# Kernel optimization log

Hardware: AMD Instinct MI355X
Metric: run time of the kernel (lower is better)

Reference implementation:

```python
import jax, jax.numpy as jnp
import numpy as np

N = 250_000          # num nodes
E = 2_000_000        # undirected edges -> 2E directed edges
C = 2                # num_class
POT = 0.95           # self potential
THRESH = 1e-6
MAX_ITERS = 10


def setup_inputs() -> dict:
    key = jax.random.key(0)
    k1, k2, k3 = jax.random.split(key, 3)
    u = jax.random.randint(k1, (E,), 0, N)
    v = jax.random.randint(k2, (E,), 0, N)
    # directed edge list: first E edges u->v, next E edges v->u
    src_nodes = jnp.concatenate([u, v]).astype(jnp.int64)
    dst_nodes = jnp.concatenate([v, u]).astype(jnp.int64)
    # reverse-edge index: edge i (<E) reverses to i+E and vice versa
    ar = jnp.arange(E, dtype=jnp.int64)
    rev_edges = jnp.concatenate([ar + E, ar])
    # strictly positive class priors, rows sum to 1
    priors = jax.nn.softmax(jax.random.normal(k3, (N, C), dtype=jnp.float32), axis=1)
    return {"priors": priors, "src_nodes": src_nodes,
            "dst_nodes": dst_nodes, "rev_edges": rev_edges}


def _potential_matrix(dtype):
    off = (1.0 - POT) / C * (C - 1)
    diag = POT / C
    P = jnp.full((C, C), off, dtype=dtype)
    return P.at[jnp.arange(C), jnp.arange(C)].set(diag)


def reference(priors, src_nodes, dst_nodes, rev_edges):
    P = _potential_matrix(priors.dtype)
    log_priors = jnp.log(priors)
    n_dir = src_nodes.shape[0]  # 2E directed edges
    messages0 = jnp.full((n_dir, C), 0.5, dtype=priors.dtype)

    def update_messages(messages, beliefs):
        # gather beliefs at edge sources, divide by reverse messages, CxC matmul
        m = (beliefs[src_nodes] / messages[rev_edges]) @ P  # [2E, C]
        return m / jnp.sum(m, axis=1, keepdims=True)

    def compute_beliefs(messages):
        b = log_priors.at[dst_nodes].add(jnp.log(messages))  # scatter-add
        return jax.nn.softmax(b, axis=1)

    def cond(state):
        i, beliefs, messages, diff = state
        return jnp.logical_and(i < MAX_ITERS, diff >= THRESH)

    def body(state):
        i, beliefs, messages, _ = state
        new_m = update_messages(messages, beliefs)
        new_b = compute_beliefs(new_m)
        diff = jnp.max(jnp.abs(new_b - beliefs))
        return (i + 1, new_b, new_m, diff)

    init = (jnp.array(0, jnp.int32), priors, messages0,
            jnp.array(jnp.inf, priors.dtype))
    _, beliefs, _, _ = jax.lax.while_loop(cond, body, init)
    return beliefs
```

## Files before the change

kernel.cpp:

```cpp
#include <hip/hip_runtime.h>
#include <hip/hip_fp16.h>


#define POT_D 0.475f
#define POT_O 0.025f

constexpr int BKT_SHIFT = 8;
constexpr int BKT_NODES = 1 << BKT_SHIFT;
constexpr int GB = 512;
constexpr int ITEMS = GB / 64;
constexpr int FB = 512;
constexpr int T = 9;

__device__ __forceinline__ float pot_logit(float x) {
  float t = __expf(-fabsf(x));
  float v = __logf((POT_D + POT_O * t) / (POT_O + POT_D * t));
  return copysignf(v, x);
}

__global__ void init_nodes(const float* __restrict__ priors, float* __restrict__ lpd, int N) {
  int n = blockIdx.x * blockDim.x + threadIdx.x;
  if (n < N) {
    float2 p = reinterpret_cast<const float2*>(priors)[n];
    lpd[n] = __logf(p.x) - __logf(p.y);
  }
}

__global__ void rank_kernel(const int* __restrict__ dst, int* __restrict__ blkhist,
                            int* __restrict__ rnk, int M, int NB, int CH) {
  extern __shared__ int h[];
  for (int i = threadIdx.x; i < NB; i += blockDim.x) h[i] = 0;
  __syncthreads();
  int s = blockIdx.x * CH, e1 = min(s + CH, M);
  for (int e = s + threadIdx.x; e < e1; e += blockDim.x)
    rnk[e] = atomicAdd(&h[dst[e] >> BKT_SHIFT], 1);
  __syncthreads();
  for (int i = threadIdx.x; i < NB; i += blockDim.x)
    blkhist[(size_t)i * GB + blockIdx.x] = h[i];
}

__global__ void colscan_kernel(int* __restrict__ blkhist, int* __restrict__ deg, int NB) {
  int wave = (blockIdx.x * blockDim.x + threadIdx.x) >> 6;
  int lane = threadIdx.x & 63;
  if (wave >= NB) return;
  int* row = blkhist + (size_t)wave * GB;
  int v[ITEMS];
  int s = 0;
#pragma unroll
  for (int j = 0; j < ITEMS; ++j) { v[j] = row[ITEMS * lane + j]; s += v[j]; }
  int tot = s;
  for (int off = 1; off < 64; off <<= 1) {
    int t = __shfl_up(tot, off, 64);
    if (lane >= off) tot += t;
  }
  int excl = tot - s;
#pragma unroll
  for (int j = 0; j < ITEMS; ++j) { int t = v[j]; row[ITEMS * lane + j] = excl; excl += t; }
  if (lane == 63) deg[wave] = tot;
}

__global__ void scan_kernel(const int* __restrict__ deg, int* __restrict__ base,
                            int NB, int M) {
  __shared__ int s[1024];
  __shared__ int carry;
  int tid = threadIdx.x;
  if (tid == 0) carry = 0;
  __syncthreads();
  for (int c = 0; c < NB; c += 1024) {
    int v = (c + tid < NB) ? deg[c + tid] : 0;
    s[tid] = v;
    __syncthreads();
    for (int off = 1; off < 1024; off <<= 1) {
      int t = (tid >= off) ? s[tid - off] : 0;
      __syncthreads();
      s[tid] += t;
      __syncthreads();
    }
    if (c + tid < NB) base[c + tid] = carry + s[tid] - v;
    __syncthreads();
    if (tid == 0) carry += s[1023];
    __syncthreads();
  }
  if (tid == 0) base[NB] = M;
}

__global__ void place_kernel(const int* __restrict__ dst, const int* __restrict__ blkhist,
                             const int* __restrict__ base, const int* __restrict__ rnk,
                             int* __restrict__ posof, int M, int NB, int CH) {
  extern __shared__ int cur[];
  for (int i = threadIdx.x; i < NB; i += blockDim.x)
    cur[i] = base[i] + blkhist[(size_t)i * GB + blockIdx.x];
  __syncthreads();
  int s = blockIdx.x * CH, e1 = min(s + CH, M);
  for (int e = s + threadIdx.x; e < e1; e += blockDim.x)
    posof[e] = cur[dst[e] >> BKT_SHIFT] + rnk[e];
}

__global__ void pass2_kernel(const int* __restrict__ dst, const int* __restrict__ posof,
                             unsigned* __restrict__ g2, int M, int E, int CH) {
  int s = blockIdx.x * CH, e1 = min(s + CH, M);
  for (int e = s + threadIdx.x; e < e1; e += blockDim.x) {
    int r = (e < E) ? (e + E) : (e - E);
    unsigned loc = (unsigned)(dst[e] & (BKT_NODES - 1));
    g2[posof[e]] = (loc << 24) | (unsigned)posof[r];
  }
}

__global__ void initcav_kernel(const unsigned* __restrict__ g2, const int* __restrict__ base,
                               const float* __restrict__ lpd, __half* __restrict__ cav) {
  int b = blockIdx.x;
  int rs = base[b], re = base[b + 1];
  for (int k = rs + threadIdx.x; k < re; k += blockDim.x) {
    int node = (b << BKT_SHIFT) | (int)(g2[k] >> 24);
    cav[k] = __float2half(lpd[node]);
  }
}

__global__ void F_kernel(const unsigned* __restrict__ g2, const int* __restrict__ base,
                         const float* __restrict__ lpd, const __half* __restrict__ cin,
                         __half* __restrict__ cout, int N) {
  __shared__ float zb[BKT_NODES];
  __shared__ float zl[BKT_NODES];
  int b = blockIdx.x;
  int rs = base[b], re = base[b + 1];
  if (threadIdx.x < BKT_NODES) zb[threadIdx.x] = 0.0f;
  __syncthreads();
  if (re > rs) {
    int k0 = rs + threadIdx.x;
    unsigned w[T];
    float L[T];
#pragma unroll
    for (int j = 0; j < T; ++j)
      w[j] = g2[min(k0 + j * FB, re - 1)];
#pragma unroll
    for (int j = 0; j < T; ++j)
      L[j] = __half2float(cin[w[j] & 0xFFFFFFu]);
#pragma unroll
    for (int j = 0; j < T; ++j) {
      L[j] = pot_logit(L[j]);
      if (k0 + j * FB < re) atomicAdd(&zb[w[j] >> 24], L[j]);
    }
    for (int k = k0 + T * FB; k < re; k += FB)
      { unsigned w2 = g2[k]; atomicAdd(&zb[w2 >> 24], pot_logit(__half2float(cin[w2 & 0xFFFFFFu]))); }
    __syncthreads();
    if (threadIdx.x < BKT_NODES) {
      int node = (b << BKT_SHIFT) + threadIdx.x;
      zl[threadIdx.x] = (node < N ? lpd[node] : 0.0f) + zb[threadIdx.x];
    }
    __syncthreads();
#pragma unroll
    for (int j = 0; j < T; ++j) {
      int k = k0 + j * FB;
      if (k < re) cout[k] = __float2half(zl[w[j] >> 24] - L[j]);
    }
    for (int k = k0 + T * FB; k < re; k += FB)
      { unsigned w2 = g2[k]; cout[k] = __float2half(zl[w2 >> 24] - pot_logit(__half2float(cin[w2 & 0xFFFFFFu]))); }
  }
}

__global__ void out_kernel(const unsigned* __restrict__ g2, const int* __restrict__ base,
                           const float* __restrict__ lpd, const __half* __restrict__ cin,
                           float2* __restrict__ out, int N) {
  __shared__ float zb[BKT_NODES];
  int b = blockIdx.x;
  int rs = base[b], re = base[b + 1];
  if (threadIdx.x < BKT_NODES) zb[threadIdx.x] = 0.0f;
  __syncthreads();
  int k0 = rs + threadIdx.x;
  if (re > rs) {
    unsigned w[T];
    float c[T];
#pragma unroll
    for (int j = 0; j < T; ++j)
      w[j] = g2[min(k0 + j * FB, re - 1)];
#pragma unroll
    for (int j = 0; j < T; ++j)
      c[j] = __half2float(cin[w[j] & 0xFFFFFFu]);
#pragma unroll
    for (int j = 0; j < T; ++j)
      if (k0 + j * FB < re) atomicAdd(&zb[w[j] >> 24], pot_logit(c[j]));
    for (int k = k0 + T * FB; k < re; k += FB)
      { unsigned w2 = g2[k]; atomicAdd(&zb[w2 >> 24], pot_logit(__half2float(cin[w2 & 0xFFFFFFu]))); }
  }
  __syncthreads();
  int node = (b << BKT_SHIFT) + threadIdx.x;
  if (threadIdx.x < BKT_NODES && node < N) {
    float z = lpd[node] + zb[threadIdx.x];
    float p = 1.0f / (1.0f + __expf(-z));
    out[node] = make_float2(p, 1.0f - p);
  }
}

extern "C" void kernel_launch(void* const* d_in, const int* in_sizes, int n_in,
                              void* d_out, int out_size, void* d_ws, size_t ws_size,
                              hipStream_t stream) {
  const float* priors = (const float*)d_in[0];
  const int* dst = (const int*)d_in[2];
  const int N = in_sizes[0] / 2;
  const int M = in_sizes[1];
  const int E = M / 2;
  const int NB = (N + BKT_NODES - 1) / BKT_NODES;
  const int CH = (M + GB - 1) / GB;

  float* ws = (float*)d_ws;
  float* lpd = ws;
  unsigned* g2 = (unsigned*)(ws + N);
  int* rnk = (int*)(ws + N + (size_t)M);
  int* posof = (int*)(ws + N + 2 * (size_t)M);
  __half* cavA = (__half*)(ws + N + 3 * (size_t)M);
  __half* cavB = cavA + M;
  int* blkhist = (int*)(ws + N + 4 * (size_t)M);
  int* deg = blkhist + (size_t)NB * GB;
  int* base = deg + NB;

  const int B = 256;
  init_nodes<<<(N + B - 1) / B, B, 0, stream>>>(priors, lpd, N);
  rank_kernel<<<GB, B, NB * sizeof(int), stream>>>(dst, blkhist, rnk, M, NB, CH);
  colscan_kernel<<<(NB * 64 + B - 1) / B, B, 0, stream>>>(blkhist, deg, NB);
  scan_kernel<<<1, 1024, 0, stream>>>(deg, base, NB, M);
  place_kernel<<<GB, B, NB * sizeof(int), stream>>>(dst, blkhist, base, rnk, posof, M, NB, CH);
  pass2_kernel<<<GB, B, 0, stream>>>(dst, posof, g2, M, E, CH);
  initcav_kernel<<<NB, B, 0, stream>>>(g2, base, lpd, cavA);

  __half* bufs[2] = {cavA, cavB};
  for (int t = 0; t < 9; ++t)
    F_kernel<<<NB, FB, 0, stream>>>(g2, base, lpd, bufs[t & 1], bufs[1 - (t & 1)], N);
  out_kernel<<<NB, FB, 0, stream>>>(g2, base, lpd, cavB, (float2*)d_out, N);
}
```

Measured before the change: 576.3 us.

## Fuse BP iterations into one persistent cooperative kernel with grid syncs

Replaces the init-cavity kernel, the nine per-iteration F kernels and the output kernel with a single cooperative kernel. It loops over buckets with a fixed grid of 512 blocks and uses grid.sync between iterations, removing repeated kernel launch overhead and tail gaps. The pass2 launch geometry is also changed to fewer, larger blocks. The cost is that each block now handles about two buckets in sequence, which gives some load imbalance. It also adds grid-wide barrier costs and the occupancy limit of a cooperative launch.

```diff
diff --git a/kernel.cpp b/kernel.cpp
--- a/kernel.cpp
+++ b/kernel.cpp
@@ -1,5 +1,8 @@
 #include <hip/hip_runtime.h>
 #include <hip/hip_fp16.h>
+#include <hip/hip_cooperative_groups.h>
+
+namespace cg = cooperative_groups;
 
 
 #define POT_D 0.475f
@@ -8,8 +11,10 @@
 constexpr int BKT_SHIFT = 8;
 constexpr int BKT_NODES = 1 << BKT_SHIFT;
 constexpr int GB = 512;
+constexpr int GB2 = 128;
 constexpr int ITEMS = GB / 64;
 constexpr int FB = 512;
+constexpr int GRID = 512;
 constexpr int T = 9;
 
 __device__ __forceinline__ float pot_logit(float x) {
@@ -97,8 +102,8 @@
 }
 
 __global__ void pass2_kernel(const int* __restrict__ dst, const int* __restrict__ posof,
-                             unsigned* __restrict__ g2, int M, int E, int CH) {
-  int s = blockIdx.x * CH, e1 = min(s + CH, M);
+                             unsigned* __restrict__ g2, int M, int E, int CH2) {
+  int s = blockIdx.x * CH2, e1 = min(s + CH2, M);
   for (int e = s + threadIdx.x; e < e1; e += blockDim.x) {
     int r = (e < E) ? (e + E) : (e - E);
     unsigned loc = (unsigned)(dst[e] & (BKT_NODES - 1));
@@ -106,88 +111,95 @@
   }
 }
 
-__global__ void initcav_kernel(const unsigned* __restrict__ g2, const int* __restrict__ base,
-                               const float* __restrict__ lpd, __half* __restrict__ cav) {
-  int b = blockIdx.x;
-  int rs = base[b], re = base[b + 1];
-  for (int k = rs + threadIdx.x; k < re; k += blockDim.x) {
-    int node = (b << BKT_SHIFT) | (int)(g2[k] >> 24);
-    cav[k] = __float2half(lpd[node]);
-  }
-}
-
-__global__ void F_kernel(const unsigned* __restrict__ g2, const int* __restrict__ base,
-                         const float* __restrict__ lpd, const __half* __restrict__ cin,
-                         __half* __restrict__ cout, int N) {
+__global__ __launch_bounds__(FB, 4) void bp_kernel(
+    const unsigned* __restrict__ g2, const int* __restrict__ base,
+    const float* __restrict__ lpd, __half* __restrict__ cavA,
+    __half* __restrict__ cavB, float2* __restrict__ out, int N, int NB) {
+  cg::grid_group grid = cg::this_grid();
   __shared__ float zb[BKT_NODES];
   __shared__ float zl[BKT_NODES];
-  int b = blockIdx.x;
-  int rs = base[b], re = base[b + 1];
-  if (threadIdx.x < BKT_NODES) zb[threadIdx.x] = 0.0f;
-  __syncthreads();
-  if (re > rs) {
-    int k0 = rs + threadIdx.x;
-    unsigned w[T];
-    float L[T];
-#pragma unroll
-    for (int j = 0; j < T; ++j)
-      w[j] = g2[min(k0 + j * FB, re - 1)];
-#pragma unroll
-    for (int j = 0; j < T; ++j)
-      L[j] = __half2float(cin[w[j] & 0xFFFFFFu]);
-#pragma unroll
-    for (int j = 0; j < T; ++j) {
-      L[j] = pot_logit(L[j]);
-      if (k0 + j * FB < re) atomicAdd(&zb[w[j] >> 24], L[j]);
-    }
-    for (int k = k0 + T * FB; k < re; k += FB)
-      { unsigned w2 = g2[k]; atomicAdd(&zb[w2 >> 24], pot_logit(__half2float(cin[w2 & 0xFFFFFFu]))); }
-    __syncthreads();
-    if (threadIdx.x < BKT_NODES) {
-      int node = (b << BKT_SHIFT) + threadIdx.x;
-      zl[threadIdx.x] = (node < N ? lpd[node] : 0.0f) + zb[threadIdx.x];
-    }
-    __syncthreads();
-#pragma unroll
-    for (int j = 0; j < T; ++j) {
-      int k = k0 + j * FB;
-      if (k < re) cout[k] = __float2half(zl[w[j] >> 24] - L[j]);
-    }
-    for (int k = k0 + T * FB; k < re; k += FB)
-      { unsigned w2 = g2[k]; cout[k] = __float2half(zl[w2 >> 24] - pot_logit(__half2float(cin[w2 & 0xFFFFFFu]))); }
-  }
-}
-
-__global__ void out_kernel(const unsigned* __restrict__ g2, const int* __restrict__ base,
-                           const float* __restrict__ lpd, const __half* __restrict__ cin,
-                           float2* __restrict__ out, int N) {
-  __shared__ float zb[BKT_NODES];
-  int b = blockIdx.x;
-  int rs = base[b], re = base[b + 1];
-  if (threadIdx.x < BKT_NODES) zb[threadIdx.x] = 0.0f;
-  __syncthreads();
-  int k0 = rs + threadIdx.x;
-  if (re > rs) {
-    unsigned w[T];
-    float c[T];
-#pragma unroll
-    for (int j = 0; j < T; ++j)
-      w[j] = g2[min(k0 + j * FB, re - 1)];
-#pragma unroll
-    for (int j = 0; j < T; ++j)
-      c[j] = __half2float(cin[w[j] & 0xFFFFFFu]);
-#pragma unroll
-    for (int j = 0; j < T; ++j)
-      if (k0 + j * FB < re) atomicAdd(&zb[w[j] >> 24], pot_logit(c[j]));
-    for (int k = k0 + T * FB; k < re; k += FB)
-      { unsigned w2 = g2[k]; atomicAdd(&zb[w2 >> 24], pot_logit(__half2float(cin[w2 & 0xFFFFFFu]))); }
-  }
-  __syncthreads();
-  int node = (b << BKT_SHIFT) + threadIdx.x;
-  if (threadIdx.x < BKT_NODES && node < N) {
-    float z = lpd[node] + zb[threadIdx.x];
-    float p = 1.0f / (1.0f + __expf(-z));
-    out[node] = make_float2(p, 1.0f - p);
+  const int tid = threadIdx.x;
+
+  for (int b = blockIdx.x; b < NB; b += gridDim.x) {
+    int rs = base[b], re = base[b + 1];
+    for (int k = rs + tid; k < re; k += FB) {
+      int node = (b << BKT_SHIFT) | (int)(g2[k] >> 24);
+      cavA[k] = __float2half(lpd[node]);
+    }
+  }
+  grid.sync();
+
+  for (int t = 1; t <= 9; ++t) {
+    const __half* cin = (t & 1) ? cavA : cavB;
+    __half* cout = (t & 1) ? cavB : cavA;
+    for (int b = blockIdx.x; b < NB; b += gridDim.x) {
+      int rs = base[b], re = base[b + 1];
+      __syncthreads();
+      if (tid < BKT_NODES) zb[tid] = 0.0f;
+      __syncthreads();
+      if (re > rs) {
+        int k0 = rs + tid;
+        unsigned w[T];
+        float L[T];
+#pragma unroll
+        for (int j = 0; j < T; ++j)
+          w[j] = g2[min(k0 + j * FB, re - 1)];
+#pragma unroll
+        for (int j = 0; j < T; ++j)
+          L[j] = __half2float(cin[w[j] & 0xFFFFFFu]);
+#pragma unroll
+        for (int j = 0; j < T; ++j) {
+          L[j] = pot_logit(L[j]);
+          if (k0 + j * FB < re) atomicAdd(&zb[w[j] >> 24], L[j]);
+        }
+        for (int k = k0 + T * FB; k < re; k += FB)
+          { unsigned w2 = g2[k]; atomicAdd(&zb[w2 >> 24], pot_logit(__half2float(cin[w2 & 0xFFFFFFu]))); }
+        __syncthreads();
+        if (tid < BKT_NODES) {
+          int node = (b << BKT_SHIFT) + tid;
+          zl[tid] = (node < N ? lpd[node] : 0.0f) + zb[tid];
+        }
+        __syncthreads();
+#pragma unroll
+        for (int j = 0; j < T; ++j) {
+          int k = k0 + j * FB;
+          if (k < re) cout[k] = __float2half(zl[w[j] >> 24] - L[j]);
+        }
+        for (int k = k0 + T * FB; k < re; k += FB)
+          { unsigned w2 = g2[k]; cout[k] = __float2half(zl[w2 >> 24] - pot_logit(__half2float(cin[w2 & 0xFFFFFFu]))); }
+      }
+    }
+    grid.sync();
+  }
+
+  for (int b = blockIdx.x; b < NB; b += gridDim.x) {
+    int rs = base[b], re = base[b + 1];
+    __syncthreads();
+    if (tid < BKT_NODES) zb[tid] = 0.0f;
+    __syncthreads();
+    if (re > rs) {
+      int k0 = rs + tid;
+      unsigned w[T];
+      float c[T];
+#pragma unroll
+      for (int j = 0; j < T; ++j)
+        w[j] = g2[min(k0 + j * FB, re - 1)];
+#pragma unroll
+      for (int j = 0; j < T; ++j)
+        c[j] = __half2float(cavB[w[j] & 0xFFFFFFu]);
+#pragma unroll
+      for (int j = 0; j < T; ++j)
+        if (k0 + j * FB < re) atomicAdd(&zb[w[j] >> 24], pot_logit(c[j]));
+      for (int k = k0 + T * FB; k < re; k += FB)
+        { unsigned w2 = g2[k]; atomicAdd(&zb[w2 >> 24], pot_logit(__half2float(cavB[w2 & 0xFFFFFFu]))); }
+    }
+    __syncthreads();
+    int node = (b << BKT_SHIFT) + tid;
+    if (tid < BKT_NODES && node < N) {
+      float z = lpd[node] + zb[tid];
+      float p = 1.0f / (1.0f + __expf(-z));
+      out[node] = make_float2(p, 1.0f - p);
+    }
   }
 }
 
@@ -196,11 +208,12 @@
                               hipStream_t stream) {
   const float* priors = (const float*)d_in[0];
   const int* dst = (const int*)d_in[2];
-  const int N = in_sizes[0] / 2;
-  const int M = in_sizes[1];
-  const int E = M / 2;
-  const int NB = (N + BKT_NODES - 1) / BKT_NODES;
-  const int CH = (M + GB - 1) / GB;
+  int N = in_sizes[0] / 2;
+  int M = in_sizes[1];
+  int E = M / 2;
+  int NB = (N + BKT_NODES - 1) / BKT_NODES;
+  int CH = (M + GB - 1) / GB;
+  int CH2 = (M + GB2 - 1) / GB2;
 
   float* ws = (float*)d_ws;
   float* lpd = ws;
@@ -212,6 +225,7 @@
   int* blkhist = (int*)(ws + N + 4 * (size_t)M);
   int* deg = blkhist + (size_t)NB * GB;
   int* base = deg + NB;
+  float2* outp = (float2*)d_out;
 
   const int B = 256;
   init_nodes<<<(N + B - 1) / B, B, 0, stream>>>(priors, lpd, N);
@@ -219,11 +233,10 @@
   colscan_kernel<<<(NB * 64 + B - 1) / B, B, 0, stream>>>(blkhist, deg, NB);
   scan_kernel<<<1, 1024, 0, stream>>>(deg, base, NB, M);
   place_kernel<<<GB, B, NB * sizeof(int), stream>>>(dst, blkhist, base, rnk, posof, M, NB, CH);
-  pass2_kernel<<<GB, B, 0, stream>>>(dst, posof, g2, M, E, CH);
-  initcav_kernel<<<NB, B, 0, stream>>>(g2, base, lpd, cavA);
-
-  __half* bufs[2] = {cavA, cavB};
-  for (int t = 0; t < 9; ++t)
-    F_kernel<<<NB, FB, 0, stream>>>(g2, base, lpd, bufs[t & 1], bufs[1 - (t & 1)], N);
-  out_kernel<<<NB, FB, 0, stream>>>(g2, base, lpd, cavB, (float2*)d_out, N);
-}
+  pass2_kernel<<<GB2, 512, 0, stream>>>(dst, posof, g2, M, E, CH2);
+
+  void* args[] = {(void*)&g2, (void*)&base, (void*)&lpd, (void*)&cavA,
+                  (void*)&cavB, (void*)&outp, (void*)&N, (void*)&NB};
+  hipLaunchCooperativeKernel(reinterpret_cast<void*>(bp_kernel),
+                             dim3(GRID), dim3(FB), args, 0, stream);
+}
```

Measured after the change: 1.203 ms. +108.8%, slower.
